# Kernel tuning notes

Hardware: AMD Instinct MI355X
Metric: run time of the kernel (lower is better)

The kernel has to match this reference:

```python
import jax, jax.numpy as jnp
import numpy as np

D_MODEL = 1024
NUM_HEADS = 16
HEAD_DIM = D_MODEL // NUM_HEADS
SCALE = HEAD_DIM ** -0.5


def _split_heads(x):
    # [B, L, D] -> [B, H, L, hd]
    B, L, _ = x.shape
    return x.reshape(B, L, NUM_HEADS, HEAD_DIM).transpose(0, 2, 1, 3)


def setup_inputs() -> dict:
    key = jax.random.key(0)
    ks = jax.random.split(key, 16)
    B, Lq, Lv, P, Lc = 8, 256, 576, 2048, 256
    inp = {
        "query_input": jax.random.normal(ks[0], (B, Lq, D_MODEL), jnp.float32),
        "visual_tokens": jax.random.normal(ks[1], (B, Lv, D_MODEL), jnp.float32),
        "past_key": jax.random.normal(ks[2], (B, NUM_HEADS, P, HEAD_DIM), jnp.float32),
        "past_value": jax.random.normal(ks[3], (B, NUM_HEADS, P, HEAD_DIM), jnp.float32),
        "past_valid_len": jax.random.randint(ks[4], (B,), 0, P + 1, jnp.int32),
        "current_context": jax.random.normal(ks[5], (B, Lc, D_MODEL), jnp.float32),
        "current_valid_mask": jax.random.randint(ks[6], (B, Lc), 0, 2, jnp.int32).astype(jnp.bool_),
    }
    s = 1.0 / np.sqrt(D_MODEL)
    inp["Wq"] = jax.random.normal(ks[7], (D_MODEL, D_MODEL), jnp.float32) * s
    inp["bq"] = jnp.zeros((D_MODEL,), jnp.float32)
    inp["Wk"] = jax.random.normal(ks[8], (D_MODEL, D_MODEL), jnp.float32) * s
    inp["bk"] = jnp.zeros((D_MODEL,), jnp.float32)
    inp["Wv"] = jax.random.normal(ks[9], (D_MODEL, D_MODEL), jnp.float32) * s
    inp["bv"] = jnp.zeros((D_MODEL,), jnp.float32)
    inp["Wo"] = jax.random.normal(ks[10], (D_MODEL, D_MODEL), jnp.float32) * s
    inp["bo"] = jnp.zeros((D_MODEL,), jnp.float32)
    return inp


def reference(query_input, visual_tokens, past_key, past_value, past_valid_len,
              current_context, current_valid_mask, Wq, bq, Wk, bk, Wv, bv, Wo, bo):
    B, Lq, _ = query_input.shape
    P = past_key.shape[2]
    Lv = visual_tokens.shape[1]
    Lc = current_context.shape[1]

    q = _split_heads(query_input @ Wq + bq)                       # [B,H,Lq,hd]
    k_vis = _split_heads(visual_tokens @ Wk + bk)                 # [B,H,Lv,hd]
    v_vis = _split_heads(visual_tokens @ Wv + bv)
    k_cur = _split_heads(current_context @ Wk + bk)               # [B,H,Lc,hd]
    v_cur = _split_heads(current_context @ Wv + bv)

    # padding masks (True = masked); full past length kept, positions >= valid_len masked
    past_mask = jnp.arange(P)[None, :] >= past_valid_len[:, None]  # [B,P]
    vis_mask = jnp.zeros((B, Lv), jnp.bool_)
    cur_mask = ~current_valid_mask                                 # [B,Lc]
    key_padding_mask = jnp.concatenate([vis_mask, past_mask, cur_mask], axis=1)  # [B,K]

    k_full = jnp.concatenate([k_vis, past_key, k_cur], axis=2)    # [B,H,K,hd]
    v_full = jnp.concatenate([v_vis, past_value, v_cur], axis=2)

    scores = jnp.einsum('bhqd,bhkd->bhqk', q, k_full) * SCALE
    neg = jnp.finfo(scores.dtype).min
    scores = jnp.where(key_padding_mask[:, None, None, :], neg, scores)
    attn = jax.nn.softmax(scores, axis=-1)
    out = jnp.einsum('bhqk,bhkd->bhqd', attn, v_full)             # [B,H,Lq,hd]
    out = out.transpose(0, 2, 1, 3).reshape(B, Lq, D_MODEL)
    return out @ Wo + bo
```

## Files before the change

### kernel.cpp

```cpp
#include <hip/hip_runtime.h>

using half8 = __attribute__((ext_vector_type(8))) _Float16;
using f32x4 = __attribute__((ext_vector_type(4))) float;

#define MFMA16(a,b,c) __builtin_amdgcn_mfma_f32_16x16x32_f16((a),(b),(c),0,0,0)

constexpr int DM = 1024;
constexpr int NH = 16;
constexpr int HD = 64;
constexpr int LQ = 256, LV = 576, PP = 2048, LC = 256;
constexpr int KVC = LV + LC;
constexpr int NSPLIT = 8;

__device__ __forceinline__ void gload16(const _Float16* g, _Float16* l) {
  __builtin_amdgcn_global_load_lds(
      (const __attribute__((address_space(1))) unsigned int*)g,
      (__attribute__((address_space(3))) unsigned int*)l,
      16, 0, 0);
}

__global__ __launch_bounds__(256) void conv_k(
    const float* __restrict__ q, const float* __restrict__ v, const float* __restrict__ c,
    _Float16* __restrict__ qo, _Float16* __restrict__ vo, _Float16* __restrict__ co)
{
  const int a = blockIdx.y;
  const float* src = a==0 ? q : a==1 ? v : c;
  _Float16*   dst  = a==0 ? qo : a==1 ? vo : co;
  const int n = (a==1) ? 8*LV*DM : 8*LQ*DM;
  const int i = (blockIdx.x*256 + threadIdx.x) * 8;
  if (i >= n) return;
  f32x4 x0 = *(const f32x4*)(src+i);
  f32x4 x1 = *(const f32x4*)(src+i+4);
  half8 y;
  #pragma unroll
  for (int j=0;j<4;++j){ y[j]=(_Float16)x0[j]; y[4+j]=(_Float16)x1[j]; }
  *(half8*)(dst+i) = y;
}

__global__ __launch_bounds__(256) void wtrans_k(
    const float* __restrict__ W0, const float* __restrict__ W1,
    const float* __restrict__ W2, const float* __restrict__ W3,
    _Float16* __restrict__ T0, _Float16* __restrict__ T1,
    _Float16* __restrict__ T2, _Float16* __restrict__ T3)
{
  __shared__ float t[64][65];
  const float* W = blockIdx.z==0 ? W0 : blockIdx.z==1 ? W1 : blockIdx.z==2 ? W2 : W3;
  _Float16*   T  = blockIdx.z==0 ? T0 : blockIdx.z==1 ? T1 : blockIdx.z==2 ? T2 : T3;
  const int k0 = blockIdx.x*64, n0 = blockIdx.y*64;
  const int r = threadIdx.x >> 2, c0 = (threadIdx.x & 3)*16;
  const float* src = W + (size_t)(k0+r)*DM + n0 + c0;
  #pragma unroll
  for (int j=0;j<4;++j) {
    f32x4 v = *(const f32x4*)(src + 4*j);
    #pragma unroll
    for (int i=0;i<4;++i) t[r][c0+4*j+i] = v[i];
  }
  __syncthreads();
  half8 o0, o1;
  #pragma unroll
  for (int i=0;i<8;++i) { o0[i] = (_Float16)t[c0+i][r]; o1[i] = (_Float16)t[c0+8+i][r]; }
  _Float16* dst = T + (size_t)(n0+r)*DM + k0 + c0;
  *(half8*)dst = o0;
  *(half8*)(dst+8) = o1;
}

template<int MODE>
__device__ __forceinline__ void gemm16_body(
    const _Float16* __restrict__ Af, const _Float16* __restrict__ Wt,
    const float* __restrict__ bias, void* __restrict__ outv,
    int L, int off, int LK, int m0, int n0)
{
  __shared__ __align__(16) _Float16 As[128*64];
  __shared__ __align__(16) _Float16 Bs[128*64];
  const int tid = threadIdx.x;
  const int lane = tid & 63, wid = tid >> 6;
  const int l15 = lane & 15, l4 = lane >> 4;
  const int wm = wid >> 1, wn = wid & 1;
  const int lrow = lane >> 3;
  const int lc8  = lane & 7;

  auto stage = [&](int kt) {
    #pragma unroll
    for (int s8 = 0; s8 < 4; ++s8) {
      const int seg = wid*4 + s8;
      const int row = seg*8 + lrow;
      const int c8  = lc8 ^ (row & 7);
      const size_t gc = (size_t)kt*64 + c8*8;
      gload16(Af + (size_t)(m0+row)*DM + gc, &As[seg*512]);
      gload16(Wt + (size_t)(n0+row)*DM + gc, &Bs[seg*512]);
    }
  };

  f32x4 acc[4][4] = {};
  stage(0);

  for (int kt=0; kt<16; ++kt) {
    __syncthreads();
    half8 af[4][2], bf[4][2];
    #pragma unroll
    for (int mf=0; mf<4; ++mf) {
      const int ra = wm*64 + mf*16 + l15;
      const int rb = wn*64 + mf*16 + l15;
      #pragma unroll
      for (int kc=0; kc<2; ++kc) {
        const int g8 = kc*4 + l4;
        af[mf][kc] = *(const half8*)&As[ra*64 + ((g8 ^ (ra&7))<<3)];
        bf[mf][kc] = *(const half8*)&Bs[rb*64 + ((g8 ^ (rb&7))<<3)];
      }
    }
    #pragma unroll
    for (int mf=0;mf<4;++mf)
      #pragma unroll
      for (int nf=0;nf<4;++nf)
        #pragma unroll
        for (int kc=0;kc<2;++kc)
          acc[mf][nf] = MFMA16(af[mf][kc], bf[nf][kc], acc[mf][nf]);
    if (kt < 15) { __syncthreads(); stage(kt+1); }
  }

  #pragma unroll
  for (int nf=0;nf<4;++nf) {
    const int col = n0 + wn*64 + nf*16 + l15;
    const float bv = bias[col];
    const int hh = col >> 6, dd = col & 63;
    #pragma unroll
    for (int mf=0;mf<4;++mf) {
      const int rbase = m0 + wm*64 + mf*16 + l4*4;
      #pragma unroll
      for (int r=0;r<4;++r) {
        const int t = rbase + r;
        const float v = acc[mf][nf][r] + bv;
        if constexpr (MODE==0) {
          const int bb = t / L, pos = t - bb*L;
          ((_Float16*)outv)[ ((size_t)((bb*NH + hh)*LK + off + pos))*HD + dd ] = (_Float16)v;
        } else {
          ((float*)outv)[ (size_t)t*DM + col ] = v;
        }
      }
    }
  }
}

__global__ __launch_bounds__(256) void proj_k(
    const _Float16* __restrict__ qf, const _Float16* __restrict__ vf, const _Float16* __restrict__ cf,
    const _Float16* __restrict__ Wtq, const _Float16* __restrict__ Wtk, const _Float16* __restrict__ Wtv,
    const float* __restrict__ bq, const float* __restrict__ bk, const float* __restrict__ bv,
    _Float16* __restrict__ qhp, _Float16* __restrict__ kvcp, _Float16* __restrict__ vvcp)
{
  const int bx = blockIdx.x, by = blockIdx.y;
  const _Float16* A; const _Float16* Wt; const float* bias; _Float16* out;
  int m0, n0, L, off, LK;
  if (bx < 16) {
    if (by >= 8) return;
    A = qf; m0 = bx*128; L = LQ; off = 0; LK = LQ;
    Wt = Wtq; bias = bq; out = qhp; n0 = by*128;
  } else {
    if (bx < 52) { A = vf; m0 = (bx-16)*128; L = LV; off = 0; }
    else         { A = cf; m0 = (bx-52)*128; L = LC; off = LV; }
    LK = KVC;
    if (by < 8) { Wt = Wtk; bias = bk; out = kvcp; n0 = by*128; }
    else        { Wt = Wtv; bias = bv; out = vvcp; n0 = (by-8)*128; }
  }
  gemm16_body<0>(A, Wt, bias, out, L, off, LK, m0, n0);
}

__global__ __launch_bounds__(256) void gemmo_k(
    const _Float16* __restrict__ A, const _Float16* __restrict__ Wt,
    const float* __restrict__ bias, float* __restrict__ out)
{
  gemm16_body<1>(A, Wt, bias, out, 1, 0, 0, blockIdx.x*128, blockIdx.y*128);
}

__global__ __launch_bounds__(512) void attn_k(
  const _Float16* __restrict__ qh, const _Float16* __restrict__ kvc,
  const _Float16* __restrict__ vvc, const float* __restrict__ pk,
  const float* __restrict__ pv, const int* __restrict__ pvl,
  const int* __restrict__ cvm, _Float16* __restrict__ Opart,
  float* __restrict__ mpart, float* __restrict__ lpart)
{
  __shared__ __align__(16) _Float16 Ks[64*72];
  __shared__ __align__(16) _Float16 Vs[64*72];
  __shared__ float mk[64];
  __shared__ __align__(16) _Float16 Ps[8][16*72];

  const int bh = blockIdx.x;
  const int ck = blockIdx.y;
  const int b = bh >> 4;
  const int tid = threadIdx.x;
  const int lane = tid & 63, wid = tid >> 6;
  const int l15 = lane & 15, l4 = lane >> 4;

  const int myvl = pvl[b];
  const int vpt = (myvl + 63) >> 6;
  const int T = 9 + vpt + 4;
  const int qn = T >> 3, rr = T & 7;
  const int len = qn + (ck < rr ? 1 : 0);
  const int lo = ck*qn + (ck < rr ? ck : rr);
  const int hi = lo + len;

  half8 aq[2][2];
  {
    const _Float16* qb = qh + ((size_t)bh*LQ + wid*32)*HD;
    #pragma unroll
    for (int rb=0;rb<2;++rb)
      #pragma unroll
      for (int kc=0;kc<2;++kc) {
        half8 x = *(const half8*)(qb + (rb*16+l15)*HD + kc*32 + l4*8);
        #pragma unroll
        for (int j=0;j<8;++j) x[j] = x[j] * (_Float16)0.125f;
        aq[rb][kc] = x;
      }
  }

  f32x4 accO[2][4] = {};
  float mrun[2][4], lrun[2][4];
  #pragma unroll
  for (int rb=0;rb<2;++rb)
    #pragma unroll
    for (int r=0;r<4;++r){ mrun[rb][r] = -3.0e38f; lrun[rb][r] = 0.f; }

  const int skey = tid >> 3;
  const int sd   = (tid & 7) * 8;
  const int vswz = (tid & 7) << 3;
  const int skeyv = skey ^ vswz;

  half8 kreg, vreg;
  f32x4 k0r, k1r, v0r, v1r;
  float mreg = 0.f;
  int ptype = 0;

  auto prefetch = [&](int t) {
    int s;
    if (t < 9)            { ptype = 0; s = t*64; }
    else if (t < 9 + vpt) { ptype = 1; s = (t-9)*64; }
    else                  { ptype = 2; s = LV + (t-9-vpt)*64; }
    if (ptype != 1) {
      const _Float16* kp = kvc + ((size_t)bh*KVC + s)*HD;
      const _Float16* vp = vvc + ((size_t)bh*KVC + s)*HD;
      kreg = *(const half8*)(kp + skey*HD + sd);
      vreg = *(const half8*)(vp + skey*HD + sd);
      if (tid < 64) mreg = (ptype==2) ? (cvm[b*LC + (s - LV) + tid] ? 0.f : -1e30f) : 0.f;
    } else {
      const float* kp = pk + ((size_t)bh*PP + s)*HD;
      const float* vp = pv + ((size_t)bh*PP + s)*HD;
      k0r = *(const f32x4*)(kp + skey*HD + sd);
      k1r = *(const f32x4*)(kp + skey*HD + sd + 4);
      v0r = *(const f32x4*)(vp + skey*HD + sd);
      v1r = *(const f32x4*)(vp + skey*HD + sd + 4);
      if (tid < 64) mreg = (s + tid < myvl) ? 0.f : -1e30f;
    }
  };

  prefetch(lo);

  for (int t=lo; t<hi; ++t) {
    __syncthreads();
    if (ptype != 1) {
      *(half8*)&Ks[skey*72 + sd] = kreg;
      #pragma unroll
      for (int j=0;j<8;++j) Vs[(sd+j)*72 + skeyv] = vreg[j];
    } else {
      half8 kx;
      #pragma unroll
      for (int i=0;i<4;++i){ kx[i] = (_Float16)k0r[i]; kx[4+i] = (_Float16)k1r[i]; }
      *(half8*)&Ks[skey*72 + sd] = kx;
      #pragma unroll
      for (int j=0;j<4;++j) Vs[(sd+j)*72 + skeyv]   = (_Float16)v0r[j];
      #pragma unroll
      for (int j=0;j<4;++j) Vs[(sd+4+j)*72 + skeyv] = (_Float16)v1r[j];
    }
    if (tid < 64) mk[tid] = mreg;
    __syncthreads();
    if (t+1 < hi) prefetch(t+1);

    half8 bk_[4][2];
    #pragma unroll
    for (int nf=0;nf<4;++nf)
      #pragma unroll
      for (int kc=0;kc<2;++kc)
        bk_[nf][kc] = *(const half8*)&Ks[(nf*16+l15)*72 + kc*32 + l4*8];
    f32x4 sf[2][4] = {};
    #pragma unroll
    for (int rb=0;rb<2;++rb)
      #pragma unroll
      for (int nf=0;nf<4;++nf)
        #pragma unroll
        for (int kc=0;kc<2;++kc)
          sf[rb][nf] = MFMA16(aq[rb][kc], bk_[nf][kc], sf[rb][nf]);

    float mc[4];
    #pragma unroll
    for (int nf=0;nf<4;++nf) mc[nf] = mk[nf*16 + l15];
    #pragma unroll
    for (int rb=0;rb<2;++rb)
      #pragma unroll
      for (int nf=0;nf<4;++nf)
        #pragma unroll
        for (int r=0;r<4;++r)
          sf[rb][nf][r] += mc[nf];

    #pragma unroll
    for (int rb=0;rb<2;++rb)
      #pragma unroll
      for (int r=0;r<4;++r) {
        float mx = fmaxf(fmaxf(sf[rb][0][r],sf[rb][1][r]), fmaxf(sf[rb][2][r],sf[rb][3][r]));
        mx = fmaxf(mx, __shfl_xor(mx,1));
        mx = fmaxf(mx, __shfl_xor(mx,2));
        mx = fmaxf(mx, __shfl_xor(mx,4));
        mx = fmaxf(mx, __shfl_xor(mx,8));
        const float mn = fmaxf(mrun[rb][r], mx);
        const float al = __expf(mrun[rb][r] - mn);
        float rs = 0.f;
        #pragma unroll
        for (int nf=0;nf<4;++nf){ float p = __expf(sf[rb][nf][r]-mn); sf[rb][nf][r]=p; rs+=p; }
        rs += __shfl_xor(rs,1);
        rs += __shfl_xor(rs,2);
        rs += __shfl_xor(rs,4);
        rs += __shfl_xor(rs,8);
        lrun[rb][r] = lrun[rb][r]*al + rs;
        mrun[rb][r] = mn;
        #pragma unroll
        for (int df=0;df<4;++df) accO[rb][df][r] *= al;
      }

    half8 bvv[4][2];
    #pragma unroll
    for (int df=0;df<4;++df) {
      const int rot = (df*2 + (l15>>3)) & 7;
      #pragma unroll
      for (int kc=0;kc<2;++kc)
        bvv[df][kc] = *(const half8*)&Vs[(df*16+l15)*72 + ((((kc<<2)|l4) ^ rot) << 3)];
    }

    _Float16* pw = &Ps[wid][0];
    #pragma unroll
    for (int rb=0;rb<2;++rb) {
      #pragma unroll
      for (int nf=0;nf<4;++nf)
        #pragma unroll
        for (int r=0;r<4;++r)
          pw[(l4*4 + r)*72 + nf*16 + l15] = (_Float16)sf[rb][nf][r];

      half8 ap[2];
      #pragma unroll
      for (int kc=0;kc<2;++kc)
        ap[kc] = *(const half8*)&pw[l15*72 + kc*32 + l4*8];

      #pragma unroll
      for (int df=0;df<4;++df)
        #pragma unroll
        for (int kc=0;kc<2;++kc)
          accO[rb][df] = MFMA16(ap[kc], bvv[df][kc], accO[rb][df]);
    }
  }

  const int base = (ck*128 + bh) * LQ;
  #pragma unroll
  for (int rb=0;rb<2;++rb)
    #pragma unroll
    for (int r=0;r<4;++r) {
      const int row = wid*32 + rb*16 + l4*4 + r;
      #pragma unroll
      for (int df=0;df<4;++df)
        Opart[((size_t)(base + row))*HD + df*16 + l15] = (_Float16)accO[rb][df][r];
      if (l15 == 0) {
        mpart[base + row] = mrun[rb][r];
        lpart[base + row] = lrun[rb][r];
      }
    }
}

__global__ __launch_bounds__(256) void combine_k(
    const _Float16* __restrict__ Opart, const float* __restrict__ mpart,
    const float* __restrict__ lpart, _Float16* __restrict__ aout)
{
  const int t = blockIdx.x*256 + threadIdx.x;
  const int rg = t >> 3;
  const int d0 = (t & 7) * 8;
  const int bh = rg >> 8, qr = rg & 255;
  const int b = bh >> 4, h = bh & 15;

  float m[NSPLIT], l[NSPLIT];
  float mstar = -3.0e38f;
  #pragma unroll
  for (int c=0;c<NSPLIT;++c) {
    m[c] = mpart[(c*128 + bh)*LQ + qr];
    l[c] = lpart[(c*128 + bh)*LQ + qr];
    mstar = fmaxf(mstar, m[c]);
  }
  float lsum = 0.f, w[NSPLIT];
  #pragma unroll
  for (int c=0;c<NSPLIT;++c) { w[c] = __expf(m[c]-mstar); lsum += l[c]*w[c]; }
  const float inv = 1.f / lsum;

  float o[8] = {};
  #pragma unroll
  for (int c=0;c<NSPLIT;++c) {
    half8 x = *(const half8*)&Opart[((size_t)((c*128 + bh)*LQ + qr))*HD + d0];
    #pragma unroll
    for (int i=0;i<8;++i) o[i] += (float)x[i]*w[c];
  }
  half8 y;
  #pragma unroll
  for (int i=0;i<8;++i) y[i] = (_Float16)(o[i]*inv);
  *(half8*)(aout + ((size_t)(b*LQ + qr))*DM + h*HD + d0) = y;
}

extern "C" void kernel_launch(void* const* d_in, const int* in_sizes, int n_in,
                              void* d_out, int out_size, void* d_ws, size_t ws_size,
                              hipStream_t stream)
{
  const float* qin = (const float*)d_in[0];
  const float* vis = (const float*)d_in[1];
  const float* pk  = (const float*)d_in[2];
  const float* pv  = (const float*)d_in[3];
  const int*   pvl = (const int*)d_in[4];
  const float* cur = (const float*)d_in[5];
  const int*   cvm = (const int*)d_in[6];
  const float* Wq = (const float*)d_in[7];  const float* bq = (const float*)d_in[8];
  const float* Wk = (const float*)d_in[9];  const float* bk = (const float*)d_in[10];
  const float* Wv = (const float*)d_in[11]; const float* bv = (const float*)d_in[12];
  const float* Wo = (const float*)d_in[13]; const float* bo = (const float*)d_in[14];

  char* ws = (char*)d_ws;
  _Float16* Wtq  = (_Float16*)(ws + ((size_t) 0<<20));
  _Float16* Wtk  = (_Float16*)(ws + ((size_t) 2<<20));
  _Float16* Wtv  = (_Float16*)(ws + ((size_t) 4<<20));
  _Float16* Wto  = (_Float16*)(ws + ((size_t) 6<<20));
  _Float16* qhp  = (_Float16*)(ws + ((size_t) 8<<20));
  _Float16* kvcp = (_Float16*)(ws + ((size_t)12<<20));
  _Float16* vvcp = (_Float16*)(ws + ((size_t)26<<20));
  _Float16* aoutp= (_Float16*)(ws + ((size_t)40<<20));
  _Float16* Opart= (_Float16*)(ws + ((size_t)45<<20));
  float*    mpart= (float*)   (ws + ((size_t)77<<20));
  float*    lpart= (float*)   (ws + ((size_t)78<<20));
  _Float16* qf16 = (_Float16*)(ws + ((size_t)45<<20));
  _Float16* vf16 = (_Float16*)(ws + ((size_t)50<<20));
  _Float16* cf16 = (_Float16*)(ws + ((size_t)60<<20));

  conv_k<<<dim3(2304,3), 256, 0, stream>>>(qin, vis, cur, qf16, vf16, cf16);

  wtrans_k<<<dim3(16,16,4), 256, 0, stream>>>(Wq,Wk,Wv,Wo, Wtq,Wtk,Wtv,Wto);

  proj_k<<<dim3(68,16), 256, 0, stream>>>(qf16, vf16, cf16, Wtq, Wtk, Wtv,
                                          bq, bk, bv, qhp, kvcp, vvcp);

  attn_k<<<dim3(128,NSPLIT), 512, 0, stream>>>(qhp, kvcp, vvcp, pk, pv, pvl, cvm,
                                               Opart, mpart, lpart);

  combine_k<<<dim3(1024), 256, 0, stream>>>(Opart, mpart, lpart, aoutp);

  gemmo_k<<<dim3(16,8), 256, 0, stream>>>(aoutp, Wto, bo, (float*)d_out);
}
```

Measured before the change: 323.8 us.

## Double-buffer K/V LDS tiles and transpose QK^T MFMA for cheaper softmax reductions

The attention kernel now keeps two LDS buffers for K, V and the mask, and writes the next tile after compute, so each iteration needs one barrier instead of two. The QK^T MFMA operands are swapped so each lane holds scores for one query row across keys. Row max and sum then take two cross-lane shuffles instead of four per register, and the probability tile is written to LDS as half4 vectors. This costs more LDS, which may lower occupancy, and adds a shuffle to broadcast the rescale factor to accumulator rows.

```diff
diff --git a/kernel.cpp b/kernel.cpp
--- a/kernel.cpp
+++ b/kernel.cpp
@@ -1,6 +1,7 @@
 #include <hip/hip_runtime.h>
 
 using half8 = __attribute__((ext_vector_type(8))) _Float16;
+using half4 = __attribute__((ext_vector_type(4))) _Float16;
 using f32x4 = __attribute__((ext_vector_type(4))) float;
 
 #define MFMA16(a,b,c) __builtin_amdgcn_mfma_f32_16x16x32_f16((a),(b),(c),0,0,0)
@@ -178,14 +179,12 @@
   const int* __restrict__ cvm, _Float16* __restrict__ Opart,
   float* __restrict__ mpart, float* __restrict__ lpart)
 {
-  __shared__ __align__(16) _Float16 Ks[64*72];
-  __shared__ __align__(16) _Float16 Vs[64*72];
-  __shared__ float mk[64];
+  __shared__ __align__(16) _Float16 Ks[2][64*72];
+  __shared__ __align__(16) _Float16 Vs[2][64*72];
+  __shared__ float mkb[2][64];
   __shared__ __align__(16) _Float16 Ps[8][16*72];
 
-  const int bh = blockIdx.x;
-  const int ck = blockIdx.y;
-  const int b = bh >> 4;
+  const int bh = blockIdx.x, ck = blockIdx.y, b = bh >> 4;
   const int tid = threadIdx.x;
   const int lane = tid & 63, wid = tid >> 6;
   const int l15 = lane & 15, l4 = lane >> 4;
@@ -213,11 +212,8 @@
   }
 
   f32x4 accO[2][4] = {};
-  float mrun[2][4], lrun[2][4];
-  #pragma unroll
-  for (int rb=0;rb<2;++rb)
-    #pragma unroll
-    for (int r=0;r<4;++r){ mrun[rb][r] = -3.0e38f; lrun[rb][r] = 0.f; }
+  float mrun2[2] = {-3.0e38f, -3.0e38f};
+  float lrun2[2] = {0.f, 0.f};
 
   const int skey = tid >> 3;
   const int sd   = (tid & 7) * 8;
@@ -251,34 +247,38 @@
     }
   };
 
-  prefetch(lo);
-
-  for (int t=lo; t<hi; ++t) {
-    __syncthreads();
+  auto writeLDS = [&](int buf) {
     if (ptype != 1) {
-      *(half8*)&Ks[skey*72 + sd] = kreg;
-      #pragma unroll
-      for (int j=0;j<8;++j) Vs[(sd+j)*72 + skeyv] = vreg[j];
+      *(half8*)&Ks[buf][skey*72 + sd] = kreg;
+      #pragma unroll
+      for (int j=0;j<8;++j) Vs[buf][(sd+j)*72 + skeyv] = vreg[j];
     } else {
       half8 kx;
       #pragma unroll
       for (int i=0;i<4;++i){ kx[i] = (_Float16)k0r[i]; kx[4+i] = (_Float16)k1r[i]; }
-      *(half8*)&Ks[skey*72 + sd] = kx;
-      #pragma unroll
-      for (int j=0;j<4;++j) Vs[(sd+j)*72 + skeyv]   = (_Float16)v0r[j];
-      #pragma unroll
-      for (int j=0;j<4;++j) Vs[(sd+4+j)*72 + skeyv] = (_Float16)v1r[j];
-    }
-    if (tid < 64) mk[tid] = mreg;
+      *(half8*)&Ks[buf][skey*72 + sd] = kx;
+      #pragma unroll
+      for (int j=0;j<4;++j) Vs[buf][(sd+j)*72 + skeyv]   = (_Float16)v0r[j];
+      #pragma unroll
+      for (int j=0;j<4;++j) Vs[buf][(sd+4+j)*72 + skeyv] = (_Float16)v1r[j];
+    }
+    if (tid < 64) mkb[buf][tid] = mreg;
+  };
+
+  prefetch(lo);
+  writeLDS(0);
+
+  for (int t=lo; t<hi; ++t) {
+    const int cur = (t - lo) & 1;
+    if (t+1 < hi) prefetch(t+1);
     __syncthreads();
-    if (t+1 < hi) prefetch(t+1);
 
     half8 bk_[4][2];
     #pragma unroll
     for (int nf=0;nf<4;++nf)
       #pragma unroll
       for (int kc=0;kc<2;++kc)
-        bk_[nf][kc] = *(const half8*)&Ks[(nf*16+l15)*72 + kc*32 + l4*8];
+        bk_[nf][kc] = *(const half8*)&Ks[cur][(nf*16+l15)*72 + kc*32 + l4*8];
     f32x4 sf[2][4] = {};
     #pragma unroll
     for (int rb=0;rb<2;++rb)
@@ -286,42 +286,7 @@
       for (int nf=0;nf<4;++nf)
         #pragma unroll
         for (int kc=0;kc<2;++kc)
-          sf[rb][nf] = MFMA16(aq[rb][kc], bk_[nf][kc], sf[rb][nf]);
-
-    float mc[4];
-    #pragma unroll
-    for (int nf=0;nf<4;++nf) mc[nf] = mk[nf*16 + l15];
-    #pragma unroll
-    for (int rb=0;rb<2;++rb)
-      #pragma unroll
-      for (int nf=0;nf<4;++nf)
-        #pragma unroll
-        for (int r=0;r<4;++r)
-          sf[rb][nf][r] += mc[nf];
-
-    #pragma unroll
-    for (int rb=0;rb<2;++rb)
-      #pragma unroll
-      for (int r=0;r<4;++r) {
-        float mx = fmaxf(fmaxf(sf[rb][0][r],sf[rb][1][r]), fmaxf(sf[rb][2][r],sf[rb][3][r]));
-        mx = fmaxf(mx, __shfl_xor(mx,1));
-        mx = fmaxf(mx, __shfl_xor(mx,2));
-        mx = fmaxf(mx, __shfl_xor(mx,4));
-        mx = fmaxf(mx, __shfl_xor(mx,8));
-        const float mn = fmaxf(mrun[rb][r], mx);
-        const float al = __expf(mrun[rb][r] - mn);
-        float rs = 0.f;
-        #pragma unroll
-        for (int nf=0;nf<4;++nf){ float p = __expf(sf[rb][nf][r]-mn); sf[rb][nf][r]=p; rs+=p; }
-        rs += __shfl_xor(rs,1);
-        rs += __shfl_xor(rs,2);
-        rs += __shfl_xor(rs,4);
-        rs += __shfl_xor(rs,8);
-        lrun[rb][r] = lrun[rb][r]*al + rs;
-        mrun[rb][r] = mn;
-        #pragma unroll
-        for (int df=0;df<4;++df) accO[rb][df][r] *= al;
-      }
+          sf[rb][nf] = MFMA16(bk_[nf][kc], aq[rb][kc], sf[rb][nf]);
 
     half8 bvv[4][2];
     #pragma unroll
@@ -329,45 +294,89 @@
       const int rot = (df*2 + (l15>>3)) & 7;
       #pragma unroll
       for (int kc=0;kc<2;++kc)
-        bvv[df][kc] = *(const half8*)&Vs[(df*16+l15)*72 + ((((kc<<2)|l4) ^ rot) << 3)];
+        bvv[df][kc] = *(const half8*)&Vs[cur][(df*16+l15)*72 + ((((kc<<2)|l4) ^ rot) << 3)];
+    }
+
+    f32x4 mc[4];
+    #pragma unroll
+    for (int nf=0;nf<4;++nf) mc[nf] = *(const f32x4*)&mkb[cur][nf*16 + l4*4];
+    #pragma unroll
+    for (int rb=0;rb<2;++rb)
+      #pragma unroll
+      for (int nf=0;nf<4;++nf)
+        sf[rb][nf] += mc[nf];
+
+    #pragma unroll
+    for (int rb=0;rb<2;++rb) {
+      float mx = sf[rb][0][0];
+      #pragma unroll
+      for (int nf=0;nf<4;++nf)
+        #pragma unroll
+        for (int r=0;r<4;++r) mx = fmaxf(mx, sf[rb][nf][r]);
+      mx = fmaxf(mx, __shfl_xor(mx, 16));
+      mx = fmaxf(mx, __shfl_xor(mx, 32));
+      const float mn = fmaxf(mrun2[rb], mx);
+      const float al = __expf(mrun2[rb] - mn);
+      float rs = 0.f;
+      #pragma unroll
+      for (int nf=0;nf<4;++nf)
+        #pragma unroll
+        for (int r=0;r<4;++r) {
+          const float p = __expf(sf[rb][nf][r] - mn);
+          sf[rb][nf][r] = p;
+          rs += p;
+        }
+      rs += __shfl_xor(rs, 16);
+      rs += __shfl_xor(rs, 32);
+      lrun2[rb] = lrun2[rb]*al + rs;
+      mrun2[rb] = mn;
+      #pragma unroll
+      for (int r=0;r<4;++r) {
+        const float alr = __shfl(al, l4*4 + r);
+        #pragma unroll
+        for (int df=0;df<4;++df) accO[rb][df][r] *= alr;
+      }
     }
 
     _Float16* pw = &Ps[wid][0];
     #pragma unroll
     for (int rb=0;rb<2;++rb) {
       #pragma unroll
-      for (int nf=0;nf<4;++nf)
-        #pragma unroll
-        for (int r=0;r<4;++r)
-          pw[(l4*4 + r)*72 + nf*16 + l15] = (_Float16)sf[rb][nf][r];
-
+      for (int nf=0;nf<4;++nf) {
+        half4 h;
+        #pragma unroll
+        for (int r=0;r<4;++r) h[r] = (_Float16)sf[rb][nf][r];
+        *(half4*)&pw[l15*72 + nf*16 + l4*4] = h;
+      }
       half8 ap[2];
       #pragma unroll
       for (int kc=0;kc<2;++kc)
         ap[kc] = *(const half8*)&pw[l15*72 + kc*32 + l4*8];
-
       #pragma unroll
       for (int df=0;df<4;++df)
         #pragma unroll
         for (int kc=0;kc<2;++kc)
           accO[rb][df] = MFMA16(ap[kc], bvv[df][kc], accO[rb][df]);
     }
+
+    if (t+1 < hi) writeLDS(cur ^ 1);
   }
 
   const int base = (ck*128 + bh) * LQ;
   #pragma unroll
-  for (int rb=0;rb<2;++rb)
+  for (int rb=0;rb<2;++rb) {
     #pragma unroll
     for (int r=0;r<4;++r) {
       const int row = wid*32 + rb*16 + l4*4 + r;
       #pragma unroll
       for (int df=0;df<4;++df)
         Opart[((size_t)(base + row))*HD + df*16 + l15] = (_Float16)accO[rb][df][r];
-      if (l15 == 0) {
-        mpart[base + row] = mrun[rb][r];
-        lpart[base + row] = lrun[rb][r];
-      }
-    }
+    }
+    if (l4 == 0) {
+      mpart[base + wid*32 + rb*16 + l15] = mrun2[rb];
+      lpart[base + wid*32 + rb*16 + l15] = lrun2[rb];
+    }
+  }
 }
 
 __global__ __launch_bounds__(256) void combine_k(
```

Result: faster. 300.4 us (-7.2%).
